# Kernel optimization log

Measured on AMD Instinct MI355X. Metric: run time of the kernel, lower is better.

## Reference

```python
import jax, jax.numpy as jnp
import numpy as np

# Config matching init_kwargs
TAUS = [0.25, 0.5, 0.75]
QWEIGHTS = [0.25, 0.5, 0.25]
T_THRESH = 10
K_DIL = 2
EPS_GIN = 0.0  # (1 + eps) * x term; train_eps=False


def setup_inputs() -> dict:
    key = jax.random.key(0)
    k0, k1, k2, k3 = jax.random.split(key, 4)
    B, N, C, H, CO = 4, 512, 64, 128, 64
    x = jax.random.normal(k0, (B, N, C), dtype=jnp.float32)
    # symmetric random binary adjacency, ~30 avg degree -> dilation active (m > T)
    u = jax.random.uniform(k1, (B, N, N))
    a = (u < 0.03).astype(jnp.float32)
    adj = jnp.maximum(a, jnp.swapaxes(a, 1, 2))
    # last 32 nodes are padding
    mask = jnp.broadcast_to(jnp.arange(N) < (N - 32), (B, N))
    W1 = jax.random.normal(k2, (C, H), dtype=jnp.float32) * (1.0 / np.sqrt(C))
    b1 = jnp.zeros((H,), dtype=jnp.float32)
    W2 = jax.random.normal(k3, (H, CO), dtype=jnp.float32) * (1.0 / np.sqrt(H))
    b2 = jnp.zeros((CO,), dtype=jnp.float32)
    return {"x": x, "adj": adj, "mask": mask, "W1": W1, "b1": b1, "W2": W2, "b2": b2}


def _dilate_adj(adj, mask):
    """Vectorized form of the per-node Python-loop dilation.
    Decisions are based on adj_ (with self-loops), exactly as in the torch loop."""
    B, N, _ = adj.shape
    eye = jnp.eye(N, dtype=bool)
    adj_ = jnp.where(eye[None], 1.0, adj)                 # add self-loops
    nb = (adj_ > 0) & (~eye)[None]                         # neighbors w/o self (B,N,N)
    m = nb.sum(-1)                                         # neighbor count (B,N)
    rank = jnp.cumsum(nb, axis=-1) - 1                     # 0-based position among neighbors
    skip = jnp.where(m > T_THRESH, (m + K_DIL - 1) // K_DIL, 1)  # ceil(m/k); linear mode, layer_idx=1
    do_dil = (skip > 1) & mask                             # masked-out rows are skipped
    removed = nb & do_dil[..., None] & (((rank + 1) % skip[..., None]) == 0)
    rem = removed | jnp.swapaxes(removed, 1, 2)            # symmetric removal
    return jnp.where(rem, 0.0, adj_)


def _weighted_nanquantile_agg(x, valid):
    """Weighted sum of linear-interpolated quantiles over the ragged neighbor dim.
    x: (B,N,C), valid: (B,N,N) bool -> (B,N,C). Empty rows -> 0 (nan_to_num)."""
    B, N, C = x.shape
    big = jnp.finfo(x.dtype).max / 4
    # pool of neighbor features, invalid slots pushed to the end of the sort
    vals = jnp.where(valid[..., None], x[:, None, :, :], big)   # (B,N,N,C)
    sv = jnp.sort(vals, axis=2)
    m = valid.sum(-1)                                           # (B,N)
    mf = m.astype(x.dtype)

    def gather(idx):  # idx (B,N) int -> (B,N,C)
        idxb = jnp.broadcast_to(idx[:, :, None, None], (B, N, 1, C))
        return jnp.take_along_axis(sv, idxb, axis=2)[:, :, 0, :]

    agg = jnp.zeros_like(x)
    for tau, wt in zip(TAUS, QWEIGHTS):
        pos = jnp.clip(tau * (mf - 1.0), 0.0)                   # torch 'linear' interpolation
        lo = jnp.floor(pos).astype(jnp.int32)
        hi = jnp.ceil(pos).astype(jnp.int32)
        frac = (pos - lo.astype(x.dtype))[..., None]
        q = gather(lo) * (1.0 - frac) + gather(hi) * frac
        agg = agg + wt * q
    return jnp.where((m > 0)[..., None], agg, 0.0)


def reference(x, adj, mask, W1, b1, W2, b2):
    dtp = x.dtype
    adj_d = _dilate_adj(adj, mask)
    agg = _weighted_nanquantile_agg(x, adj_d > 0)
    out = (1.0 + EPS_GIN) * x + agg
    h = jax.nn.relu(jnp.einsum('bnc,ch->bnh', out, W1) + b1)    # GIN MLP
    y = jnp.einsum('bnh,ho->bno', h, W2) + b2
    return y * mask[..., None].astype(dtp)
```

## Files before the change

kernel.cpp:

```cpp
#include <hip/hip_runtime.h>
#include <stdint.h>

#define NB 4
#define NN 512
#define NC 64
#define NH 128
#define NCO 64
#define MAXM 64
#define STR 17

__device__ inline bool read_mask(const void* mp, int idx) {
    const int* ip = (const int*)mp;
    int w0 = ip[0];
    if (w0 == 1) return ip[idx] != 0;
    if (w0 == 0x3f800000) return ((const float*)mp)[idx] != 0.0f;
    return ((const unsigned char*)mp)[idx] != 0;
}

__global__ __launch_bounds__(256) void prep_kernel(
        const float* __restrict__ adj, const void* __restrict__ maskp,
        const float* __restrict__ W1, const float* __restrict__ W2,
        uint64_t* __restrict__ rembits, float* __restrict__ W1T,
        float* __restrict__ W2T, int dowt)
{
    int wave = (blockIdx.x * 256 + threadIdx.x) >> 6;
    int lane = threadIdx.x & 63;
    if (wave < NB * NN) {
        int i = wave & (NN - 1);
        const float* arow = adj + (size_t)wave * NN;
        uint64_t ball[8];
        int m = 0;
        #pragma unroll
        for (int k = 0; k < 8; ++k) {
            int j = k * 64 + lane;
            bool f = (j != i) && (arow[j] > 0.0f);
            uint64_t bl = __ballot(f);
            ball[k] = bl;
            m += __popcll(bl);
        }
        int skip = (m > 10) ? ((m + 1) >> 1) : 1;
        bool dodil = (skip > 1) && read_mask(maskp, wave);
        int skip2 = skip * 2;
        int prefix = 0;
        #pragma unroll
        for (int k = 0; k < 8; ++k) {
            uint64_t bl = ball[k];
            int rank1 = prefix + __popcll(bl & ((1ull << lane) - 1ull)) + 1;
            bool f = (bl >> lane) & 1ull;
            bool rm = f && dodil && (rank1 == skip || rank1 == skip2);
            uint64_t rb = __ballot(rm);
            if (lane == 0) rembits[(size_t)wave * 8 + k] = rb;
            prefix += __popcll(bl);
        }
    }
    if (dowt) {
        int e = blockIdx.x * 256 + threadIdx.x;
        if (e < 8192) {
            int k = e >> 6, c = e & 63;
            W1T[e] = W1[c * NH + k];
        } else if (e < 16384) {
            int e2 = e - 8192;
            int o = e2 >> 7, k = e2 & 127;
            W2T[e2] = W2[k * NCO + o];
        }
    }
}

template<bool USE_WT>
__global__ __launch_bounds__(256) void fused_kernel(
        const float* __restrict__ x,
        const float* __restrict__ adj,
        const void* __restrict__ maskp,
        const float* __restrict__ W1,
        const float* __restrict__ b1,
        const float* __restrict__ W2,
        const float* __restrict__ b2,
        const uint64_t* __restrict__ rembits,
        const float* __restrict__ W1T,
        const float* __restrict__ W2T,
        float* __restrict__ out)
{
    int row = blockIdx.x;
    int b = row >> 9, i = row & (NN - 1);
    int tid = threadIdx.x, lane = tid & 63, wv = tid >> 6;
    float* outp = out + (size_t)row * NCO;

    if (!read_mask(maskp, row)) {
        if (tid < NCO) outp[tid] = 0.0f;
        return;
    }

    __shared__ int s_idx[NN];
    __shared__ int s_cnt;
    __shared__ float4 s_q4[NC * STR];
    __shared__ float s_qv[NC * 8];
    __shared__ float s_out[NC];
    __shared__ float s_h[NH];
    __shared__ float s_hp[2][NH];
    __shared__ float s_part[4][NCO];

    float xval = (tid < NC) ? x[(size_t)row * NC + tid] : 0.0f;
    if (tid == 0) s_cnt = 0;
    __syncthreads();

    const float* arow = adj + (size_t)row * NN;
    const uint64_t* remI = rembits + (size_t)row * 8;
    int ic = i >> 6, ibit = i & 63;
    #pragma unroll
    for (int it = 0; it < 2; ++it) {
        int j = tid + it * 256;
        float a = arow[j];
        uint64_t wI = remI[j >> 6];
        uint64_t wJ = rembits[((size_t)(b * NN + j)) * 8 + ic];
        bool valid = (j == i) ||
                     ((a > 0.0f) && !((wI >> (j & 63)) & 1ull)
                                 && !((wJ >> ibit) & 1ull));
        if (valid) {
            int p = atomicAdd(&s_cnt, 1);
            s_idx[p] = j;
        }
    }
    __syncthreads();
    int m = s_cnt;

    float* sv = (float*)s_q4;
    bool fast = (m <= MAXM);
    int mq = (m + 3) >> 2;
    if (fast) {
        int mq4 = mq << 2;
        for (int t = tid; t < mq4 * 64; t += 256) {
            int j = t >> 6, c = t & 63;
            float v = 3.0e38f;
            if (j < m) v = x[((size_t)(b * NN + s_idx[j])) * NC + c];
            sv[c * 68 + j] = v;
        }
    }
    __syncthreads();

    float mf = (float)m;
    const float taus[3] = {0.25f, 0.5f, 0.75f};
    const float wts[3]  = {0.25f, 0.5f, 0.25f};
    int tlo[3], thi[3];
    float tfrac[3];
    #pragma unroll
    for (int t = 0; t < 3; ++t) {
        float pos = taus[t] * (mf - 1.0f);
        float fl = floorf(pos);
        tlo[t] = (int)fl;
        thi[t] = (int)ceilf(pos);
        tfrac[t] = pos - fl;
    }

    int c = lane;
    if (fast) {
        const float4* basep = s_q4 + c * STR;
        for (int ch = wv; ch < mq; ch += 4) {
            float4 q1 = basep[ch];
            int rs0 = 0, rs1 = 0, rs2 = 0, rs3 = 0;
            int re0 = 0, re1 = 0, re2 = 0, re3 = 0;
            for (int jq = 0; jq < mq; ++jq) {
                float4 v = basep[jq];
                rs0 += (v.x < q1.x) + (v.y < q1.x) + (v.z < q1.x) + (v.w < q1.x);
                re0 += (v.x == q1.x) + (v.y == q1.x) + (v.z == q1.x) + (v.w == q1.x);
                rs1 += (v.x < q1.y) + (v.y < q1.y) + (v.z < q1.y) + (v.w < q1.y);
                re1 += (v.x == q1.y) + (v.y == q1.y) + (v.z == q1.y) + (v.w == q1.y);
                rs2 += (v.x < q1.z) + (v.y < q1.z) + (v.z < q1.z) + (v.w < q1.z);
                re2 += (v.x == q1.z) + (v.y == q1.z) + (v.z == q1.z) + (v.w == q1.z);
                rs3 += (v.x < q1.w) + (v.y < q1.w) + (v.z < q1.w) + (v.w < q1.w);
                re3 += (v.x == q1.w) + (v.y == q1.w) + (v.z == q1.w) + (v.w == q1.w);
            }
            float qe[4] = {q1.x, q1.y, q1.z, q1.w};
            int rsa[4] = {rs0, rs1, rs2, rs3};
            int rea[4] = {re0, re1, re2, re3};
            #pragma unroll
            for (int q = 0; q < 4; ++q) {
                #pragma unroll
                for (int t = 0; t < 3; ++t) {
                    if (rsa[q] <= tlo[t] && tlo[t] < rsa[q] + rea[q])
                        s_qv[c * 8 + 2 * t] = qe[q];
                    if (rsa[q] <= thi[t] && thi[t] < rsa[q] + rea[q])
                        s_qv[c * 8 + 2 * t + 1] = qe[q];
                }
            }
        }
    } else if (tid < NC) {
        const float* xb = x + (size_t)b * NN * NC;
        for (int j1 = 0; j1 < m; ++j1) {
            float v1 = xb[(size_t)s_idx[j1] * NC + c];
            int rs = 0, re = 0;
            for (int j2 = 0; j2 < m; ++j2) {
                float v2 = xb[(size_t)s_idx[j2] * NC + c];
                rs += v2 < v1;
                re += v2 == v1;
            }
            #pragma unroll
            for (int t = 0; t < 3; ++t) {
                if (rs <= tlo[t] && tlo[t] < rs + re) s_qv[c * 8 + 2 * t] = v1;
                if (rs <= thi[t] && thi[t] < rs + re) s_qv[c * 8 + 2 * t + 1] = v1;
            }
        }
    }
    __syncthreads();

    if (tid < NC) {
        float agg = 0.0f;
        #pragma unroll
        for (int t = 0; t < 3; ++t) {
            float q = s_qv[tid * 8 + 2 * t] * (1.0f - tfrac[t])
                    + s_qv[tid * 8 + 2 * t + 1] * tfrac[t];
            agg += wts[t] * q;
        }
        s_out[tid] = xval + agg;
    }
    __syncthreads();

    {
        int k = tid & 127, g = tid >> 7;
        float acc = 0.0f;
        if (USE_WT) {
            const float4* w = (const float4*)(W1T + k * 64 + g * 32);
            #pragma unroll
            for (int q = 0; q < 8; ++q) {
                float4 wq = w[q];
                int cc = g * 32 + q * 4;
                acc += wq.x * s_out[cc] + wq.y * s_out[cc + 1]
                     + wq.z * s_out[cc + 2] + wq.w * s_out[cc + 3];
            }
        } else {
            for (int cc = g * 32; cc < g * 32 + 32; ++cc)
                acc += s_out[cc] * W1[cc * NH + k];
        }
        s_hp[g][k] = acc;
    }
    __syncthreads();
    if (tid < NH) {
        float acc = s_hp[0][tid] + s_hp[1][tid] + b1[tid];
        s_h[tid] = acc > 0.0f ? acc : 0.0f;
    }
    __syncthreads();

    {
        int o = tid & 63, g = tid >> 6;
        float acc = 0.0f;
        if (USE_WT) {
            const float4* w = (const float4*)(W2T + o * 128 + g * 32);
            #pragma unroll
            for (int q = 0; q < 8; ++q) {
                float4 wq = w[q];
                int k = g * 32 + q * 4;
                acc += wq.x * s_h[k] + wq.y * s_h[k + 1]
                     + wq.z * s_h[k + 2] + wq.w * s_h[k + 3];
            }
        } else {
            for (int k = g * 32; k < g * 32 + 32; ++k)
                acc += s_h[k] * W2[k * NCO + o];
        }
        s_part[g][o] = acc;
    }
    __syncthreads();
    if (tid < NCO)
        outp[tid] = s_part[0][tid] + s_part[1][tid] + s_part[2][tid]
                  + s_part[3][tid] + b2[tid];
}

extern "C" void kernel_launch(void* const* d_in, const int* in_sizes, int n_in,
                              void* d_out, int out_size, void* d_ws, size_t ws_size,
                              hipStream_t stream) {
    const float* x   = (const float*)d_in[0];
    const float* adj = (const float*)d_in[1];
    const void* mask = d_in[2];
    const float* W1  = (const float*)d_in[3];
    const float* b1  = (const float*)d_in[4];
    const float* W2  = (const float*)d_in[5];
    const float* b2  = (const float*)d_in[6];
    float* out = (float*)d_out;

    uint64_t* rembits = (uint64_t*)d_ws;
    float* W1T = (float*)((char*)d_ws + 131072);
    float* W2T = W1T + 8192;
    int dowt = (ws_size >= 196608) ? 1 : 0;

    prep_kernel<<<512, 256, 0, stream>>>(adj, mask, W1, W2, rembits, W1T, W2T, dowt);
    if (dowt)
        fused_kernel<true><<<NB * NN, 256, 0, stream>>>(
            x, adj, mask, W1, b1, W2, b2, rembits, W1T, W2T, out);
    else
        fused_kernel<false><<<NB * NN, 256, 0, stream>>>(
            x, adj, mask, W1, b1, W2, b2, rembits, W1T, W2T, out);
}
```

Before: 107.5 us.

## Store kept-neighbor bitmasks and drop dense adjacency reads in fused kernel

The prep kernel now writes bitmasks of kept neighbors instead of removed ones. The fused kernel builds its neighbor list from these bits and no longer reads the dense adjacency row, so it fetches the transposed word only for candidate neighbors. Shared memory shrinks: indices become 16-bit, the padded stride is replaced by an XOR swizzle, and the MLP scratch buffers reuse the sort buffer. A launch-bounds occupancy hint is added. The cost is more index arithmetic in the sort loops and a tighter register budget.

```diff
diff --git a/kernel.cpp b/kernel.cpp
--- a/kernel.cpp
+++ b/kernel.cpp
@@ -7,7 +7,7 @@
 #define NH 128
 #define NCO 64
 #define MAXM 64
-#define STR 17
+#define MAXQ 16
 
 __device__ inline bool read_mask(const void* mp, int idx) {
     const int* ip = (const int*)mp;
@@ -20,7 +20,7 @@
 __global__ __launch_bounds__(256) void prep_kernel(
         const float* __restrict__ adj, const void* __restrict__ maskp,
         const float* __restrict__ W1, const float* __restrict__ W2,
-        uint64_t* __restrict__ rembits, float* __restrict__ W1T,
+        uint64_t* __restrict__ validbits, float* __restrict__ W1T,
         float* __restrict__ W2T, int dowt)
 {
     int wave = (blockIdx.x * 256 + threadIdx.x) >> 6;
@@ -47,9 +47,9 @@
             uint64_t bl = ball[k];
             int rank1 = prefix + __popcll(bl & ((1ull << lane) - 1ull)) + 1;
             bool f = (bl >> lane) & 1ull;
-            bool rm = f && dodil && (rank1 == skip || rank1 == skip2);
-            uint64_t rb = __ballot(rm);
-            if (lane == 0) rembits[(size_t)wave * 8 + k] = rb;
+            bool keep = f && !(dodil && (rank1 == skip || rank1 == skip2));
+            uint64_t vb = __ballot(keep);
+            if (lane == 0) validbits[(size_t)wave * 8 + k] = vb;
             prefix += __popcll(bl);
         }
     }
@@ -67,15 +67,14 @@
 }
 
 template<bool USE_WT>
-__global__ __launch_bounds__(256) void fused_kernel(
+__global__ __launch_bounds__(256, 8) void fused_kernel(
         const float* __restrict__ x,
-        const float* __restrict__ adj,
         const void* __restrict__ maskp,
         const float* __restrict__ W1,
         const float* __restrict__ b1,
         const float* __restrict__ W2,
         const float* __restrict__ b2,
-        const uint64_t* __restrict__ rembits,
+        const uint64_t* __restrict__ validbits,
         const float* __restrict__ W1T,
         const float* __restrict__ W2T,
         float* __restrict__ out)
@@ -90,49 +89,43 @@
         return;
     }
 
-    __shared__ int s_idx[NN];
+    __shared__ float4 s_q4[NC * MAXQ];
+    __shared__ uint16_t s_idx[NN];
+    __shared__ float s_qv[NC * 8];
+    __shared__ uint64_t s_vb[8];
     __shared__ int s_cnt;
-    __shared__ float4 s_q4[NC * STR];
-    __shared__ float s_qv[NC * 8];
-    __shared__ float s_out[NC];
-    __shared__ float s_h[NH];
-    __shared__ float s_hp[2][NH];
-    __shared__ float s_part[4][NCO];
 
     float xval = (tid < NC) ? x[(size_t)row * NC + tid] : 0.0f;
-    if (tid == 0) s_cnt = 0;
-    __syncthreads();
-
-    const float* arow = adj + (size_t)row * NN;
-    const uint64_t* remI = rembits + (size_t)row * 8;
-    int ic = i >> 6, ibit = i & 63;
+    if (tid < 8) s_vb[tid] = validbits[(size_t)row * 8 + tid];
+    if (tid == 0) { s_cnt = 1; s_idx[0] = (uint16_t)i; }
+    __syncthreads();
+
+    int ic = i >> 6;
+    uint64_t imask = 1ull << (i & 63);
     #pragma unroll
     for (int it = 0; it < 2; ++it) {
         int j = tid + it * 256;
-        float a = arow[j];
-        uint64_t wI = remI[j >> 6];
-        uint64_t wJ = rembits[((size_t)(b * NN + j)) * 8 + ic];
-        bool valid = (j == i) ||
-                     ((a > 0.0f) && !((wI >> (j & 63)) & 1ull)
-                                 && !((wJ >> ibit) & 1ull));
-        if (valid) {
-            int p = atomicAdd(&s_cnt, 1);
-            s_idx[p] = j;
+        if ((s_vb[j >> 6] >> (j & 63)) & 1ull) {
+            uint64_t wJ = validbits[((size_t)(b * NN + j)) * 8 + ic];
+            if (wJ & imask) {
+                int p = atomicAdd(&s_cnt, 1);
+                s_idx[p] = (uint16_t)j;
+            }
         }
     }
     __syncthreads();
     int m = s_cnt;
 
-    float* sv = (float*)s_q4;
     bool fast = (m <= MAXM);
     int mq = (m + 3) >> 2;
+    float* sv = (float*)s_q4;
     if (fast) {
         int mq4 = mq << 2;
-        for (int t = tid; t < mq4 * 64; t += 256) {
-            int j = t >> 6, c = t & 63;
+        for (int j = wv; j < mq4; j += 4) {
             float v = 3.0e38f;
-            if (j < m) v = x[((size_t)(b * NN + s_idx[j])) * NC + c];
-            sv[c * 68 + j] = v;
+            if (j < m) v = x[((size_t)(b * NN + s_idx[j])) * NC + lane];
+            int slot = (j >> 2) ^ (lane & 15);
+            sv[lane * 64 + slot * 4 + (j & 3)] = v;
         }
     }
     __syncthreads();
@@ -151,15 +144,15 @@
         tfrac[t] = pos - fl;
     }
 
-    int c = lane;
     if (fast) {
-        const float4* basep = s_q4 + c * STR;
+        const float4* basep = s_q4 + lane * MAXQ;
+        int sw = lane & 15;
         for (int ch = wv; ch < mq; ch += 4) {
-            float4 q1 = basep[ch];
+            float4 q1 = basep[ch ^ sw];
             int rs0 = 0, rs1 = 0, rs2 = 0, rs3 = 0;
             int re0 = 0, re1 = 0, re2 = 0, re3 = 0;
             for (int jq = 0; jq < mq; ++jq) {
-                float4 v = basep[jq];
+                float4 v = basep[jq ^ sw];
                 rs0 += (v.x < q1.x) + (v.y < q1.x) + (v.z < q1.x) + (v.w < q1.x);
                 re0 += (v.x == q1.x) + (v.y == q1.x) + (v.z == q1.x) + (v.w == q1.x);
                 rs1 += (v.x < q1.y) + (v.y < q1.y) + (v.z < q1.y) + (v.w < q1.y);
@@ -177,14 +170,15 @@
                 #pragma unroll
                 for (int t = 0; t < 3; ++t) {
                     if (rsa[q] <= tlo[t] && tlo[t] < rsa[q] + rea[q])
-                        s_qv[c * 8 + 2 * t] = qe[q];
+                        s_qv[lane * 8 + 2 * t] = qe[q];
                     if (rsa[q] <= thi[t] && thi[t] < rsa[q] + rea[q])
-                        s_qv[c * 8 + 2 * t + 1] = qe[q];
+                        s_qv[lane * 8 + 2 * t + 1] = qe[q];
                 }
             }
         }
     } else if (tid < NC) {
         const float* xb = x + (size_t)b * NN * NC;
+        int c = tid;
         for (int j1 = 0; j1 < m; ++j1) {
             float v1 = xb[(size_t)s_idx[j1] * NC + c];
             int rs = 0, re = 0;
@@ -202,6 +196,12 @@
     }
     __syncthreads();
 
+    float* s_mlp  = (float*)s_q4;
+    float* s_out  = s_mlp;
+    float* s_h    = s_mlp + 64;
+    float* s_hp   = s_mlp + 256;
+    float* s_part = s_mlp + 512;
+
     if (tid < NC) {
         float agg = 0.0f;
         #pragma unroll
@@ -230,12 +230,12 @@
             for (int cc = g * 32; cc < g * 32 + 32; ++cc)
                 acc += s_out[cc] * W1[cc * NH + k];
         }
-        s_hp[g][k] = acc;
+        s_hp[g * NH + k] = acc;
     }
     __syncthreads();
     if (tid < NH) {
-        float acc = s_hp[0][tid] + s_hp[1][tid] + b1[tid];
-        s_h[tid] = acc > 0.0f ? acc : 0.0f;
+        float a = s_hp[tid] + s_hp[NH + tid] + b1[tid];
+        s_h[tid] = a > 0.0f ? a : 0.0f;
     }
     __syncthreads();
 
@@ -255,12 +255,12 @@
             for (int k = g * 32; k < g * 32 + 32; ++k)
                 acc += s_h[k] * W2[k * NCO + o];
         }
-        s_part[g][o] = acc;
+        s_part[g * NCO + o] = acc;
     }
     __syncthreads();
     if (tid < NCO)
-        outp[tid] = s_part[0][tid] + s_part[1][tid] + s_part[2][tid]
-                  + s_part[3][tid] + b2[tid];
+        outp[tid] = s_part[tid] + s_part[64 + tid] + s_part[128 + tid]
+                  + s_part[192 + tid] + b2[tid];
 }
 
 extern "C" void kernel_launch(void* const* d_in, const int* in_sizes, int n_in,
@@ -275,16 +275,16 @@
     const float* b2  = (const float*)d_in[6];
     float* out = (float*)d_out;
 
-    uint64_t* rembits = (uint64_t*)d_ws;
+    uint64_t* validbits = (uint64_t*)d_ws;
     float* W1T = (float*)((char*)d_ws + 131072);
     float* W2T = W1T + 8192;
     int dowt = (ws_size >= 196608) ? 1 : 0;
 
-    prep_kernel<<<512, 256, 0, stream>>>(adj, mask, W1, W2, rembits, W1T, W2T, dowt);
+    prep_kernel<<<512, 256, 0, stream>>>(adj, mask, W1, W2, validbits, W1T, W2T, dowt);
     if (dowt)
         fused_kernel<true><<<NB * NN, 256, 0, stream>>>(
-            x, adj, mask, W1, b1, W2, b2, rembits, W1T, W2T, out);
+            x, mask, W1, b1, W2, b2, validbits, W1T, W2T, out);
     else
         fused_kernel<false><<<NB * NN, 256, 0, stream>>>(
-            x, adj, mask, W1, b1, W2, b2, rembits, W1T, W2T, out);
-}
+            x, mask, W1, b1, W2, b2, validbits, W1T, W2T, out);
+}
```

After: 103.5 us. 1.04x faster.
